# Optimization experiments

Hardware: AMD Instinct MI355X
Metric: run time of the kernel (lower is better)

## Reference

```python
import jax, jax.numpy as jnp
import numpy as np

T, B, D_IN, D_LAT, D_OUT = 512, 256, 256, 512, 256

def setup_inputs() -> dict:
    key = jax.random.key(0)
    k = jax.random.split(key, 4)
    scale_h = 1.0 / np.sqrt(D_IN + D_LAT)
    scale_o = 1.0 / np.sqrt(D_LAT)
    return {
        "x": jax.random.normal(k[0], (T, B, D_IN), dtype=jnp.float32),
        "h": jnp.zeros((B, D_LAT), dtype=jnp.float32),
        "Wh": jax.random.normal(k[1], (D_IN + D_LAT, D_LAT), dtype=jnp.float32) * scale_h,
        "bh": jnp.zeros((D_LAT,), dtype=jnp.float32),
        "Wo": jax.random.normal(k[2], (D_LAT, D_OUT), dtype=jnp.float32) * scale_o,
        "bo": jnp.zeros((D_OUT,), dtype=jnp.float32),
    }

def reference(x, h, Wh, bh, Wo, bo):
    # Split Wh into input / hidden blocks: cat(x,h) @ Wh == x@Wx + h@Wr
    Wx = Wh[:D_IN]    # [D_IN, D_LAT]
    Wr = Wh[D_IN:]    # [D_LAT, D_LAT]

    def step(h_prev, x_t):
        h_next = jax.nn.relu(x_t @ Wx + h_prev @ Wr + bh)  # [B, D_LAT]
        return h_next, h_next

    _, hidden_states = jax.lax.scan(step, h, x)            # [T, B, D_LAT]
    outputs = hidden_states @ Wo + bo                      # [T, B, D_OUT]
    return outputs, hidden_states
```

## Files before the change

kernel.cpp:

```cpp
#include <hip/hip_runtime.h>
#include <hip/hip_bf16.h>


#define TT 512
#define BB 256
#define DIN 256
#define DLAT 512
#define DOUT 256

typedef short bf16x8 __attribute__((ext_vector_type(8)));
typedef int   i32x4  __attribute__((ext_vector_type(4)));
typedef float f32x4  __attribute__((ext_vector_type(4)));

__device__ __forceinline__ unsigned short f2bf(float f) {
  union { float f; unsigned u; } v; v.f = f;
  unsigned r = v.u + (((v.u >> 16) & 1u) + 0x7fffu);
  return (unsigned short)(r >> 16);
}
__device__ __forceinline__ unsigned pack2(float a, float b) {
  return (unsigned)f2bf(a) | ((unsigned)f2bf(b) << 16);
}

__device__ __forceinline__ i32x4 load_b128_sc(const void* p) {
  i32x4 r;
  asm volatile("global_load_dwordx4 %0, %1, off sc0 sc1" : "=v"(r) : "v"(p) : "memory");
  return r;
}
__device__ __forceinline__ void store_b128_sc(void* p, i32x4 v) {
  asm volatile("global_store_dwordx4 %0, %1, off sc0 sc1" :: "v"(p), "v"(v) : "memory");
}
__device__ __forceinline__ void store_flag_sc(void* p, int v) {
  asm volatile("global_store_dword %0, %1, off sc0 sc1" :: "v"(p), "v"(v) : "memory");
}
__device__ __forceinline__ int load_flag_sc(const void* p) {
  int r;
  asm volatile("global_load_dword %0, %1, off sc0 sc1\n\ts_waitcnt vmcnt(0)"
               : "=v"(r) : "v"(p) : "memory");
  return r;
}
__device__ __forceinline__ void waitvm0() {
  asm volatile("s_waitcnt vmcnt(0)" ::: "memory");
  __builtin_amdgcn_sched_barrier(0);
}
__device__ __forceinline__ void waitvm6() {
  asm volatile("s_waitcnt vmcnt(6)" ::: "memory");
  __builtin_amdgcn_sched_barrier(0);
}

__global__ __launch_bounds__(256) void prep_kernel(
    const float* __restrict__ Wh, const float* __restrict__ Wo,
    unsigned short* __restrict__ wx, unsigned short* __restrict__ wr,
    unsigned short* __restrict__ wo) {
  int id = blockIdx.x * 256 + threadIdx.x;
  {
    int k = id >> 9, col = id & 511;
    int s = col >> 7, c = col & 127;
    wr[(s << 16) + (((c << 9) | k) ^ ((c & 7) << 3))] = f2bf(Wh[(256 + k) * 512 + col]);
  }
  if (id < 131072) {
    int k = id >> 9, col = id & 511;
    int s = col >> 7, c = col & 127;
    wx[(s << 15) + (((c << 8) | k) ^ ((c & 7) << 3))] = f2bf(Wh[id]);
  }
  if (id < 131072) {
    int k = id >> 8, col = id & 255;
    int s = col >> 7, c = col & 127;
    wo[(s << 16) + (((c << 9) | k) ^ ((c & 7) << 3))] = f2bf(Wo[id]);
  }
}

template <int K, int NSTR, int SLBITS>
__global__ __launch_bounds__(256) void gemm_bias(
    const float* __restrict__ Xg, const unsigned short* __restrict__ Wp,
    const float* __restrict__ bias, float* __restrict__ Cg) {
  __shared__ unsigned short ldsW[128 * K];
  __shared__ unsigned short ldsA[128 * 64];
  const int tid = threadIdx.x;
  const int s = blockIdx.x & ((1 << SLBITS) - 1);
  const size_t r0 = (size_t)(blockIdx.x >> SLBITS) * 128;
  {
    const uint4* src = (const uint4*)(Wp + (size_t)s * 128 * K);
    uint4* dst = (uint4*)ldsW;
#pragma unroll
    for (int i = 0; i < (128 * K / 8) / 256; ++i) dst[tid + 256 * i] = src[tid + 256 * i];
  }
  const int lane = tid & 63, wid = tid >> 6;
  const int wm = wid >> 1, wn = wid & 1;
  const int cl = lane & 15, kh = lane >> 4;
  f32x4 acc[4][4];
#pragma unroll
  for (int nf = 0; nf < 4; ++nf) {
    float bv = bias[s * 128 + wn * 64 + nf * 16 + cl];
#pragma unroll
    for (int mf = 0; mf < 4; ++mf) { f32x4 t = {bv, bv, bv, bv}; acc[mf][nf] = t; }
  }
  __syncthreads();
  for (int k0 = 0; k0 < K; k0 += 64) {
#pragma unroll
    for (int i = 0; i < 8; ++i) {
      int g = tid + 256 * i;
      int row = g >> 4, kg = g & 15;
      const float4 v = *(const float4*)&Xg[(r0 + row) * K + (k0 + kg * 4)];
      int idx = (row * 64 + kg * 4) ^ ((row & 7) << 3);
      uint2 u; u.x = pack2(v.x, v.y); u.y = pack2(v.z, v.w);
      *(uint2*)&ldsA[idx] = u;
    }
    __syncthreads();
#pragma unroll
    for (int kk = 0; kk < 2; ++kk) {
      bf16x8 aF[4], bF[4];
#pragma unroll
      for (int mf = 0; mf < 4; ++mf) {
        int row = wm * 64 + mf * 16 + cl;
        int kl = kk * 32 + 8 * kh;
        aF[mf] = *(const bf16x8*)&ldsA[(row * 64 + kl) ^ ((row & 7) << 3)];
      }
#pragma unroll
      for (int nf = 0; nf < 4; ++nf) {
        int cc = wn * 64 + nf * 16 + cl;
        int k = k0 + kk * 32 + 8 * kh;
        bF[nf] = *(const bf16x8*)&ldsW[(cc * K + k) ^ ((cc & 7) << 3)];
      }
#pragma unroll
      for (int mf = 0; mf < 4; ++mf)
#pragma unroll
        for (int nf = 0; nf < 4; ++nf)
          acc[mf][nf] = __builtin_amdgcn_mfma_f32_16x16x32_bf16(aF[mf], bF[nf], acc[mf][nf], 0, 0, 0);
    }
    __syncthreads();
  }
#pragma unroll
  for (int mf = 0; mf < 4; ++mf)
#pragma unroll
    for (int nf = 0; nf < 4; ++nf)
#pragma unroll
      for (int j = 0; j < 4; ++j)
        Cg[(r0 + wm * 64 + mf * 16 + kh * 4 + j) * NSTR + s * 128 + wn * 64 + nf * 16 + cl] =
            acc[mf][nf][j];
}

__global__ __launch_bounds__(256) void scan_kernel(
    const float* __restrict__ h0, const unsigned short* __restrict__ WrP,
    float* __restrict__ Hid, int* __restrict__ flags, unsigned short* __restrict__ ex) {
  __shared__ unsigned short lt[16][136];
  const int tid = threadIdx.x, lane = tid & 63, wid = tid >> 6;
  const int g = blockIdx.x & 15, c = blockIdx.x >> 4;
  const int r0 = g * 16;
  const int c0 = c * 128;
  const int cl = lane & 15, kh = lane >> 4;
  const int wc = c0 + wid * 32;
  int* flags4 = flags + g * 4;

  bf16x8 bwR0[16], bwR1[16];
  {
    const unsigned short* base = WrP + (size_t)c * 65536;
    const int cb0 = wid * 32 + cl, cb1 = cb0 + 16;
#pragma unroll
    for (int i = 0; i < 16; ++i) {
      int kk = (c * 4 + i) & 15;
      int k = kk * 32 + 8 * kh;
      bwR0[i] = *(const bf16x8*)(base + (((cb0 << 9) | k) ^ ((cb0 & 7) << 3)));
      bwR1[i] = *(const bf16x8*)(base + (((cb1 << 9) | k) ^ ((cb1 & 7) << 3)));
    }
  }

  {
    int r = tid >> 4, cb = (tid & 15) * 8;
    const float* hs = h0 + (size_t)(r0 + r) * DLAT + c0 + cb;
    float4 a = *(const float4*)&hs[0];
    float4 b = *(const float4*)&hs[4];
    i32x4 w;
    w[0] = (int)pack2(a.x, a.y); w[1] = (int)pack2(a.z, a.w);
    w[2] = (int)pack2(b.x, b.y); w[3] = (int)pack2(b.z, b.w);
    *(i32x4*)&lt[r][cb] = w;
    store_b128_sc(ex + (size_t)(16 + g) * 8192 + r * 512 + c0 + cb, w);
    waitvm0();
  }
  __syncthreads();
  if (tid == 0) store_flag_sc(&flags4[c], 0);

  for (int t = 0; t < TT; ++t) {
    float ai0[4], ai1[4];
    const float* At = Hid + (size_t)t * (BB * DLAT);
#pragma unroll
    for (int j = 0; j < 4; ++j) {
      ai0[j] = At[(r0 + kh * 4 + j) * DLAT + wc + cl];
      ai1[j] = At[(r0 + kh * 4 + j) * DLAT + wc + 16 + cl];
    }
    i32x4 of[4];
#pragma unroll
    for (int i = 0; i < 4; ++i) of[i] = *(const i32x4*)&lt[cl][i * 32 + kh * 8];
    if (tid < 4) {
      while (load_flag_sc(&flags4[tid]) < t) {}
    }
    __syncthreads();

    f32x4 acc0 = {ai0[0], ai0[1], ai0[2], ai0[3]};
    f32x4 acc1 = {ai1[0], ai1[1], ai1[2], ai1[3]};
    __builtin_amdgcn_sched_barrier(0);

    const unsigned short* exR = ex + (size_t)(((t + 1) & 1) * 16 + g) * 8192;
    i32x4 fa[12];
#pragma unroll
    for (int i = 0; i < 12; ++i) {
      int kk = (c * 4 + 4 + i) & 15;
      fa[i] = load_b128_sc(exR + cl * 512 + kk * 32 + kh * 8);
    }
#pragma unroll
    for (int i = 0; i < 4; ++i) {
      bf16x8 aF = __builtin_bit_cast(bf16x8, of[i]);
      acc0 = __builtin_amdgcn_mfma_f32_16x16x32_bf16(aF, bwR0[i], acc0, 0, 0, 0);
      acc1 = __builtin_amdgcn_mfma_f32_16x16x32_bf16(aF, bwR1[i], acc1, 0, 0, 0);
    }
    waitvm6();
#pragma unroll
    for (int i = 0; i < 6; ++i) {
      bf16x8 aF = __builtin_bit_cast(bf16x8, fa[i]);
      acc0 = __builtin_amdgcn_mfma_f32_16x16x32_bf16(aF, bwR0[4 + i], acc0, 0, 0, 0);
      acc1 = __builtin_amdgcn_mfma_f32_16x16x32_bf16(aF, bwR1[4 + i], acc1, 0, 0, 0);
    }
    waitvm0();
#pragma unroll
    for (int i = 6; i < 12; ++i) {
      bf16x8 aF = __builtin_bit_cast(bf16x8, fa[i]);
      acc0 = __builtin_amdgcn_mfma_f32_16x16x32_bf16(aF, bwR0[4 + i], acc0, 0, 0, 0);
      acc1 = __builtin_amdgcn_mfma_f32_16x16x32_bf16(aF, bwR1[4 + i], acc1, 0, 0, 0);
    }

    float v0[4], v1[4];
#pragma unroll
    for (int j = 0; j < 4; ++j) {
      v0[j] = fmaxf(acc0[j], 0.f);
      v1[j] = fmaxf(acc1[j], 0.f);
      lt[kh * 4 + j][wid * 32 + cl] = f2bf(v0[j]);
      lt[kh * 4 + j][wid * 32 + 16 + cl] = f2bf(v1[j]);
    }
    if (t < TT - 1) {
      __syncthreads();
      int r = tid >> 4, cb = (tid & 15) * 8;
      i32x4 w = *(const i32x4*)&lt[r][cb];
      store_b128_sc(ex + (size_t)((t & 1) * 16 + g) * 8192 + r * 512 + c0 + cb, w);
      waitvm0();
      __syncthreads();
      if (tid == 0) store_flag_sc(&flags4[c], t + 1);
    }
    float* Ht = Hid + (size_t)t * (BB * DLAT);
#pragma unroll
    for (int j = 0; j < 4; ++j) {
      Ht[(r0 + kh * 4 + j) * DLAT + wc + cl] = v0[j];
      Ht[(r0 + kh * 4 + j) * DLAT + wc + 16 + cl] = v1[j];
    }
  }
}

extern "C" void kernel_launch(void* const* d_in, const int* in_sizes, int n_in,
                              void* d_out, int out_size, void* d_ws, size_t ws_size,
                              hipStream_t stream) {
  const float* x  = (const float*)d_in[0];
  const float* h0 = (const float*)d_in[1];
  const float* Wh = (const float*)d_in[2];
  const float* bh = (const float*)d_in[3];
  const float* Wo = (const float*)d_in[4];
  const float* bo = (const float*)d_in[5];
  float* Out = (float*)d_out;
  float* Hid = Out + (size_t)TT * BB * DOUT;

  unsigned short* ws_wx = (unsigned short*)d_ws;
  unsigned short* ws_wr = ws_wx + 131072;
  unsigned short* ws_wo = ws_wr + 262144;
  int* flags = (int*)(ws_wo + 131072);
  unsigned short* ex = (unsigned short*)(flags + 64);

  hipMemsetAsync(flags, 0xFF, 64 * sizeof(int), stream);
  prep_kernel<<<1024, 256, 0, stream>>>(Wh, Wo, ws_wx, ws_wr, ws_wo);
  gemm_bias<256, 512, 2><<<4096, 256, 0, stream>>>(x, ws_wx, bh, Hid);
  scan_kernel<<<64, 256, 0, stream>>>(h0, ws_wr, Hid, flags, ex);
  gemm_bias<512, 256, 1><<<2048, 256, 0, stream>>>(Hid, ws_wo, bo, Out);
}
```

Measured before the change: 2.285 ms.

## Replace flag-based inter-block sync with sign-bit polarity tagged data exchange

Removes the per-step flag store and flag polling in the recurrent scan. Consumers instead spin on the exchanged bf16 hidden-state data itself, with the sign bit carrying a step-parity polarity. This is safe because ReLU outputs are non-negative. Step 0 is peeled to use h0 directly, and the precomputed input projection for the next step is prefetched one iteration ahead. The cost is extra masking work and repeated loads while spinning, plus a larger memset of the exchange buffer.

```diff
diff --git a/kernel.cpp b/kernel.cpp
--- a/kernel.cpp
+++ b/kernel.cpp
@@ -29,22 +29,14 @@
 __device__ __forceinline__ void store_b128_sc(void* p, i32x4 v) {
   asm volatile("global_store_dwordx4 %0, %1, off sc0 sc1" :: "v"(p), "v"(v) : "memory");
 }
-__device__ __forceinline__ void store_flag_sc(void* p, int v) {
-  asm volatile("global_store_dword %0, %1, off sc0 sc1" :: "v"(p), "v"(v) : "memory");
-}
-__device__ __forceinline__ int load_flag_sc(const void* p) {
-  int r;
-  asm volatile("global_load_dword %0, %1, off sc0 sc1\n\ts_waitcnt vmcnt(0)"
-               : "=v"(r) : "v"(p) : "memory");
-  return r;
-}
 __device__ __forceinline__ void waitvm0() {
   asm volatile("s_waitcnt vmcnt(0)" ::: "memory");
   __builtin_amdgcn_sched_barrier(0);
 }
-__device__ __forceinline__ void waitvm6() {
-  asm volatile("s_waitcnt vmcnt(6)" ::: "memory");
-  __builtin_amdgcn_sched_barrier(0);
+__device__ __forceinline__ i32x4 load_b128_pin(const void* p) {
+  i32x4 r;
+  asm volatile("global_load_dwordx4 %0, %1, off" : "=v"(r) : "v"(p) : "memory");
+  return r;
 }
 
 __global__ __launch_bounds__(256) void prep_kernel(
@@ -139,19 +131,18 @@
             acc[mf][nf][j];
 }
 
-__global__ __launch_bounds__(256) void scan_kernel(
+__global__ __launch_bounds__(256, 1) void scan_kernel(
     const float* __restrict__ h0, const unsigned short* __restrict__ WrP,
-    float* __restrict__ Hid, int* __restrict__ flags, unsigned short* __restrict__ ex) {
+    float* __restrict__ Hid, unsigned short* __restrict__ ex) {
   __shared__ unsigned short lt[16][136];
   const int tid = threadIdx.x, lane = tid & 63, wid = tid >> 6;
   const int g = blockIdx.x & 15, c = blockIdx.x >> 4;
-  const int r0 = g * 16;
-  const int c0 = c * 128;
+  const int r0 = g * 16, c0 = c * 128;
   const int cl = lane & 15, kh = lane >> 4;
   const int wc = c0 + wid * 32;
-  int* flags4 = flags + g * 4;
-
-  bf16x8 bwR0[16], bwR1[16];
+  const int xr = tid >> 4, xcb = (tid & 15) * 8;
+
+  i32x4 bwR0[16], bwR1[16];
   {
     const unsigned short* base = WrP + (size_t)c * 65536;
     const int cb0 = wid * 32 + cl, cb1 = cb0 + 16;
@@ -159,90 +150,129 @@
     for (int i = 0; i < 16; ++i) {
       int kk = (c * 4 + i) & 15;
       int k = kk * 32 + 8 * kh;
-      bwR0[i] = *(const bf16x8*)(base + (((cb0 << 9) | k) ^ ((cb0 & 7) << 3)));
-      bwR1[i] = *(const bf16x8*)(base + (((cb1 << 9) | k) ^ ((cb1 & 7) << 3)));
-    }
-  }
-
-  {
-    int r = tid >> 4, cb = (tid & 15) * 8;
-    const float* hs = h0 + (size_t)(r0 + r) * DLAT + c0 + cb;
-    float4 a = *(const float4*)&hs[0];
-    float4 b = *(const float4*)&hs[4];
+      bwR0[i] = load_b128_pin(base + (((cb0 << 9) | k) ^ ((cb0 & 7) << 3)));
+      bwR1[i] = load_b128_pin(base + (((cb1 << 9) | k) ^ ((cb1 & 7) << 3)));
+    }
+    waitvm0();
+  }
+
+  float ai0[4], ai1[4];
+#pragma unroll
+  for (int j = 0; j < 4; ++j) {
+    ai0[j] = Hid[(r0 + kh * 4 + j) * DLAT + wc + cl];
+    ai1[j] = Hid[(r0 + kh * 4 + j) * DLAT + wc + 16 + cl];
+  }
+  f32x4 acc0 = {ai0[0], ai0[1], ai0[2], ai0[3]};
+  f32x4 acc1 = {ai1[0], ai1[1], ai1[2], ai1[3]};
+#pragma unroll
+  for (int i = 0; i < 16; ++i) {
+    int kk = (c * 4 + i) & 15;
+    const float* hp = h0 + (size_t)(r0 + cl) * DLAT + kk * 32 + kh * 8;
+    float4 a = *(const float4*)hp;
+    float4 b = *(const float4*)(hp + 4);
     i32x4 w;
     w[0] = (int)pack2(a.x, a.y); w[1] = (int)pack2(a.z, a.w);
     w[2] = (int)pack2(b.x, b.y); w[3] = (int)pack2(b.z, b.w);
-    *(i32x4*)&lt[r][cb] = w;
-    store_b128_sc(ex + (size_t)(16 + g) * 8192 + r * 512 + c0 + cb, w);
-    waitvm0();
-  }
-  __syncthreads();
-  if (tid == 0) store_flag_sc(&flags4[c], 0);
-
-  for (int t = 0; t < TT; ++t) {
-    float ai0[4], ai1[4];
-    const float* At = Hid + (size_t)t * (BB * DLAT);
-#pragma unroll
-    for (int j = 0; j < 4; ++j) {
-      ai0[j] = At[(r0 + kh * 4 + j) * DLAT + wc + cl];
-      ai1[j] = At[(r0 + kh * 4 + j) * DLAT + wc + 16 + cl];
-    }
+    bf16x8 aF = __builtin_bit_cast(bf16x8, w);
+    acc0 = __builtin_amdgcn_mfma_f32_16x16x32_bf16(aF, __builtin_bit_cast(bf16x8, bwR0[i]), acc0, 0, 0, 0);
+    acc1 = __builtin_amdgcn_mfma_f32_16x16x32_bf16(aF, __builtin_bit_cast(bf16x8, bwR1[i]), acc1, 0, 0, 0);
+  }
+  {
+    float v0[4], v1[4];
+#pragma unroll
+    for (int j = 0; j < 4; ++j) {
+      v0[j] = fmaxf(acc0[j], 0.f);
+      v1[j] = fmaxf(acc1[j], 0.f);
+      lt[kh * 4 + j][wid * 32 + cl] = (unsigned short)(f2bf(v0[j]) & 0x7fff);
+      lt[kh * 4 + j][wid * 32 + 16 + cl] = (unsigned short)(f2bf(v1[j]) & 0x7fff);
+    }
+    __syncthreads();
+    i32x4 w = *(const i32x4*)&lt[xr][xcb];
+    store_b128_sc(ex + (size_t)g * 8192 + xr * 512 + c0 + xcb, w);
+#pragma unroll
+    for (int j = 0; j < 4; ++j) {
+      Hid[(r0 + kh * 4 + j) * DLAT + wc + cl] = v0[j];
+      Hid[(r0 + kh * 4 + j) * DLAT + wc + 16 + cl] = v1[j];
+    }
+    const float* An = Hid + (size_t)1 * (BB * DLAT);
+#pragma unroll
+    for (int j = 0; j < 4; ++j) {
+      ai0[j] = An[(r0 + kh * 4 + j) * DLAT + wc + cl];
+      ai1[j] = An[(r0 + kh * 4 + j) * DLAT + wc + 16 + cl];
+    }
+  }
+
+  for (int t = 1; t < TT; ++t) {
     i32x4 of[4];
 #pragma unroll
     for (int i = 0; i < 4; ++i) of[i] = *(const i32x4*)&lt[cl][i * 32 + kh * 8];
-    if (tid < 4) {
-      while (load_flag_sc(&flags4[tid]) < t) {}
-    }
-    __syncthreads();
-
-    f32x4 acc0 = {ai0[0], ai0[1], ai0[2], ai0[3]};
-    f32x4 acc1 = {ai1[0], ai1[1], ai1[2], ai1[3]};
-    __builtin_amdgcn_sched_barrier(0);
-
-    const unsigned short* exR = ex + (size_t)(((t + 1) & 1) * 16 + g) * 8192;
-    i32x4 fa[12];
-#pragma unroll
-    for (int i = 0; i < 12; ++i) {
-      int kk = (c * 4 + 4 + i) & 15;
-      fa[i] = load_b128_sc(exR + cl * 512 + kk * 32 + kh * 8);
-    }
+    __syncthreads();
+
+    f32x4 a0 = {ai0[0], ai0[1], ai0[2], ai0[3]};
+    f32x4 a1 = {ai1[0], ai1[1], ai1[2], ai1[3]};
 #pragma unroll
     for (int i = 0; i < 4; ++i) {
       bf16x8 aF = __builtin_bit_cast(bf16x8, of[i]);
-      acc0 = __builtin_amdgcn_mfma_f32_16x16x32_bf16(aF, bwR0[i], acc0, 0, 0, 0);
-      acc1 = __builtin_amdgcn_mfma_f32_16x16x32_bf16(aF, bwR1[i], acc1, 0, 0, 0);
-    }
-    waitvm6();
-#pragma unroll
-    for (int i = 0; i < 6; ++i) {
-      bf16x8 aF = __builtin_bit_cast(bf16x8, fa[i]);
-      acc0 = __builtin_amdgcn_mfma_f32_16x16x32_bf16(aF, bwR0[4 + i], acc0, 0, 0, 0);
-      acc1 = __builtin_amdgcn_mfma_f32_16x16x32_bf16(aF, bwR1[4 + i], acc1, 0, 0, 0);
-    }
-    waitvm0();
-#pragma unroll
-    for (int i = 6; i < 12; ++i) {
-      bf16x8 aF = __builtin_bit_cast(bf16x8, fa[i]);
-      acc0 = __builtin_amdgcn_mfma_f32_16x16x32_bf16(aF, bwR0[4 + i], acc0, 0, 0, 0);
-      acc1 = __builtin_amdgcn_mfma_f32_16x16x32_bf16(aF, bwR1[4 + i], acc1, 0, 0, 0);
+      a0 = __builtin_amdgcn_mfma_f32_16x16x32_bf16(aF, __builtin_bit_cast(bf16x8, bwR0[i]), a0, 0, 0, 0);
+      a1 = __builtin_amdgcn_mfma_f32_16x16x32_bf16(aF, __builtin_bit_cast(bf16x8, bwR1[i]), a1, 0, 0, 0);
+    }
+
+    const unsigned short* exR = ex + (size_t)((t - 1) & 1) * 131072 + (size_t)g * 8192;
+    const unsigned polr = (((t - 1) >> 1) & 1) ? 0x80008000u : 0u;
+    i32x4 fa[12];
+    for (;;) {
+#pragma unroll
+      for (int i = 0; i < 12; ++i) {
+        int kk = (c * 4 + 4 + i) & 15;
+        fa[i] = load_b128_sc(exR + cl * 512 + kk * 32 + kh * 8);
+      }
+      waitvm0();
+      unsigned bad = 0;
+#pragma unroll
+      for (int i = 0; i < 12; ++i)
+#pragma unroll
+        for (int q = 0; q < 4; ++q)
+          bad |= ((unsigned)fa[i][q] ^ polr) & 0x80008000u;
+      if (!__any(bad)) break;
+    }
+
+    float an0[4], an1[4];
+    {
+      int tn = (t < TT - 1) ? t + 1 : TT - 1;
+      const float* An = Hid + (size_t)tn * (BB * DLAT);
+#pragma unroll
+      for (int j = 0; j < 4; ++j) {
+        an0[j] = An[(r0 + kh * 4 + j) * DLAT + wc + cl];
+        an1[j] = An[(r0 + kh * 4 + j) * DLAT + wc + 16 + cl];
+      }
+    }
+
+#pragma unroll
+    for (int i = 0; i < 12; ++i) {
+      i32x4 w = fa[i];
+#pragma unroll
+      for (int q = 0; q < 4; ++q) w[q] = (int)((unsigned)w[q] & 0x7fff7fffu);
+      bf16x8 aF = __builtin_bit_cast(bf16x8, w);
+      a0 = __builtin_amdgcn_mfma_f32_16x16x32_bf16(aF, __builtin_bit_cast(bf16x8, bwR0[4 + i]), a0, 0, 0, 0);
+      a1 = __builtin_amdgcn_mfma_f32_16x16x32_bf16(aF, __builtin_bit_cast(bf16x8, bwR1[4 + i]), a1, 0, 0, 0);
     }
 
     float v0[4], v1[4];
 #pragma unroll
     for (int j = 0; j < 4; ++j) {
-      v0[j] = fmaxf(acc0[j], 0.f);
-      v1[j] = fmaxf(acc1[j], 0.f);
-      lt[kh * 4 + j][wid * 32 + cl] = f2bf(v0[j]);
-      lt[kh * 4 + j][wid * 32 + 16 + cl] = f2bf(v1[j]);
-    }
+      v0[j] = fmaxf(a0[j], 0.f);
+      v1[j] = fmaxf(a1[j], 0.f);
+      lt[kh * 4 + j][wid * 32 + cl] = (unsigned short)(f2bf(v0[j]) & 0x7fff);
+      lt[kh * 4 + j][wid * 32 + 16 + cl] = (unsigned short)(f2bf(v1[j]) & 0x7fff);
+    }
+    __syncthreads();
+
     if (t < TT - 1) {
-      __syncthreads();
-      int r = tid >> 4, cb = (tid & 15) * 8;
-      i32x4 w = *(const i32x4*)&lt[r][cb];
-      store_b128_sc(ex + (size_t)((t & 1) * 16 + g) * 8192 + r * 512 + c0 + cb, w);
-      waitvm0();
-      __syncthreads();
-      if (tid == 0) store_flag_sc(&flags4[c], t + 1);
+      i32x4 w = *(const i32x4*)&lt[xr][xcb];
+      const unsigned polw = ((t >> 1) & 1) ? 0x80008000u : 0u;
+#pragma unroll
+      for (int q = 0; q < 4; ++q) w[q] = (int)((unsigned)w[q] | polw);
+      store_b128_sc(ex + (size_t)(t & 1) * 131072 + (size_t)g * 8192 + xr * 512 + c0 + xcb, w);
     }
     float* Ht = Hid + (size_t)t * (BB * DLAT);
 #pragma unroll
@@ -250,6 +280,8 @@
       Ht[(r0 + kh * 4 + j) * DLAT + wc + cl] = v0[j];
       Ht[(r0 + kh * 4 + j) * DLAT + wc + 16 + cl] = v1[j];
     }
+#pragma unroll
+    for (int j = 0; j < 4; ++j) { ai0[j] = an0[j]; ai1[j] = an1[j]; }
   }
 }
 
@@ -268,12 +300,11 @@
   unsigned short* ws_wx = (unsigned short*)d_ws;
   unsigned short* ws_wr = ws_wx + 131072;
   unsigned short* ws_wo = ws_wr + 262144;
-  int* flags = (int*)(ws_wo + 131072);
-  unsigned short* ex = (unsigned short*)(flags + 64);
-
-  hipMemsetAsync(flags, 0xFF, 64 * sizeof(int), stream);
+  unsigned short* ex = ws_wo + 131072;
+
+  hipMemsetAsync(ex, 0xFF, 2 * 131072 * sizeof(unsigned short), stream);
   prep_kernel<<<1024, 256, 0, stream>>>(Wh, Wo, ws_wx, ws_wr, ws_wo);
   gemm_bias<256, 512, 2><<<4096, 256, 0, stream>>>(x, ws_wx, bh, Hid);
-  scan_kernel<<<64, 256, 0, stream>>>(h0, ws_wr, Hid, flags, ex);
+  scan_kernel<<<64, 256, 0, stream>>>(h0, ws_wr, Hid, ex);
   gemm_bias<512, 256, 1><<<2048, 256, 0, stream>>>(Hid, ws_wo, bo, Out);
 }
```

Measured after the change: 2.452 ms. 1.07x slower.
